# Performance work log

Measured on AMD Instinct MI355X. Metric: run time of the kernel, lower is better.

## Reference

```python
import jax, jax.numpy as jnp
import numpy as np

LN_EPS = 1e-5


def _ln(x, g, b):
    mu = jnp.mean(x, -1, keepdims=True)
    xc = x - mu
    inv = jax.lax.rsqrt(jnp.mean(xc * xc, -1, keepdims=True) + LN_EPS)
    return xc * inv * g + b


def _subm_conv(x, nbr, W, b):
    # Submanifold 3D conv via rulebook gather-GEMM-accumulate.
    # x: [N, Cin], nbr: [N, K] neighbor row ids (-1 = missing), W: [K, Cin, Cout], b: [Cout]
    N = x.shape[0]
    xp = jnp.concatenate([x, jnp.zeros((1, x.shape[1]), x.dtype)], 0)  # sentinel zero row
    idx = jnp.where(nbr < 0, N, nbr)  # missing neighbors -> zero row
    acc0 = jnp.zeros((N, W.shape[-1]), x.dtype) + b
    def body(acc, xs):
        i, Wk = xs  # i: [N], Wk: [Cin, Cout]
        return acc + xp[i] @ Wk, None
    acc, _ = jax.lax.scan(body, acc0, (idx.T, W))
    return acc


def _blk1(x, W, b, g, be):  # 1x1x1 SubMConv + LN + ReLU
    return jax.nn.relu(_ln(x @ W + b, g, be))


def _blk3(x, nbr, W, b, g, be):  # 3x3x3 SubMConv + LN + ReLU
    return jax.nn.relu(_ln(_subm_conv(x, nbr, W, b), g, be))


def setup_inputs() -> dict:
    rng = np.random.default_rng(0)
    B, D, Npb, K = 2, 160, 131072, 27
    dim, half = 64, 32
    # Build random sparse voxel set and the rulebook (neighbor table) like spconv does.
    lookup = np.full((B, D, D, D), -1, np.int64)
    coords = np.zeros((B * Npb, 3), np.int64)
    for b in range(B):
        lin = np.sort(rng.choice(D * D * D, size=Npb, replace=False))
        z, y, x = np.unravel_index(lin, (D, D, D))
        rows = np.arange(b * Npb, (b + 1) * Npb)
        lookup[b, z, y, x] = rows
        coords[rows] = np.stack([z, y, x], 1)
    bidx = np.repeat(np.arange(B), Npb)
    offs = np.stack(np.meshgrid(np.arange(-1, 2), np.arange(-1, 2), np.arange(-1, 2), indexing="ij"), -1).reshape(K, 3)
    nz = coords[:, None, :] + offs[None]  # [N, K, 3]
    valid = ((nz >= 0) & (nz < D)).all(-1)
    nzc = np.clip(nz, 0, D - 1)
    nbr = lookup[bidx[:, None], nzc[..., 0], nzc[..., 1], nzc[..., 2]]
    nbr = np.where(valid, nbr, -1).astype(np.int32)

    key = jax.random.key(0)
    ks = iter(jax.random.split(key, 16))
    f32 = jnp.float32
    d = {"voxel_features": jax.random.normal(next(ks), (B * Npb, dim), f32),
         "nbr_idx": jnp.asarray(nbr)}
    def lnp(c):
        return jnp.ones((c,), f32), jnp.zeros((c,), f32)
    d["W1"] = 0.05 * jax.random.normal(next(ks), (dim, dim), f32); d["b1"] = jnp.zeros((dim,), f32); d["g1"], d["be1"] = lnp(dim)
    d["W2"] = 0.05 * jax.random.normal(next(ks), (dim, dim), f32); d["b2"] = jnp.zeros((dim,), f32); d["g2"], d["be2"] = lnp(dim)
    d["W3"] = 0.05 * jax.random.normal(next(ks), (K, dim, half), f32); d["b3"] = jnp.zeros((half,), f32); d["g3"], d["be3"] = lnp(half)
    d["W4"] = 0.05 * jax.random.normal(next(ks), (K, half, half), f32); d["b4"] = jnp.zeros((half,), f32); d["g4"], d["be4"] = lnp(half)
    d["W5"] = 0.05 * jax.random.normal(next(ks), (K, half, half), f32); d["b5"] = jnp.zeros((half,), f32); d["g5"], d["be5"] = lnp(half)
    d["W6"] = 0.05 * jax.random.normal(next(ks), (K, half, half), f32); d["b6"] = jnp.zeros((half,), f32); d["g6"], d["be6"] = lnp(half)
    d["W7"] = 0.05 * jax.random.normal(next(ks), (4 * dim, dim), f32); d["b7"] = jnp.zeros((dim,), f32); d["g7"], d["be7"] = lnp(dim)
    return d


def reference(voxel_features, nbr_idx,
              W1, b1, g1, be1, W2, b2, g2, be2,
              W3, b3, g3, be3, W4, b4, g4, be4,
              W5, b5, g5, be5, W6, b6, g6, be6,
              W7, b7, g7, be7):
    x = voxel_features
    f1 = _blk1(x, W1, b1, g1, be1)
    f2 = _blk1(x, W2, b2, g2, be2)
    feats = [f1, f2]
    f2 = _blk3(f2, nbr_idx, W3, b3, g3, be3); feats.append(f2)
    f2 = _blk3(f2, nbr_idx, W4, b4, g4, be4); feats.append(f2)
    f2 = _blk3(f2, nbr_idx, W5, b5, g5, be5); feats.append(f2)
    f2 = _blk3(f2, nbr_idx, W6, b6, g6, be6); feats.append(f2)
    cat = jnp.concatenate(feats, -1)  # [N, 4*dim]
    return _blk1(cat, W7, b7, g7, be7)
```

## Files before the change

kernel.cpp:

```cpp
#include <hip/hip_runtime.h>

typedef __attribute__((ext_vector_type(4))) float  float4_;
typedef __attribute__((ext_vector_type(8))) short  short8;
typedef __attribute__((ext_vector_type(8))) __bf16 bf16x8;

__device__ inline unsigned short f2bf(float f) {
    unsigned u = __builtin_bit_cast(unsigned, f);
    u += 0x7FFFu + ((u >> 16) & 1u);
    return (unsigned short)(u >> 16);
}

__device__ inline float4_ mfma16(bf16x8 a, bf16x8 b, float4_ c) {
    return __builtin_amdgcn_mfma_f32_16x16x32_bf16(a, b, c, 0, 0, 0);
}

__device__ inline void packW_one(const float* __restrict__ src, unsigned short* __restrict__ dst,
                                 int cin, int cout, int e) {
    int f = e >> 9, i = e & 511, lane = i >> 3, t = i & 7;
    int ntn = cout >> 4, ctn = cin >> 5;
    int nt = f % ntn;
    int rest = f / ntn;
    int ct = rest % ctn;
    int k = rest / ctn;
    int c = ct * 32 + (lane >> 4) * 8 + t;
    int j = nt * 16 + (lane & 15);
    dst[e] = f2bf(src[(k * cin + c) * cout + j]);
}

__global__ void pack_all_kernel(
    const float* __restrict__ W1, const float* __restrict__ W2,
    const float* __restrict__ W3, const float* __restrict__ W4,
    const float* __restrict__ W5, const float* __restrict__ W6,
    const float* __restrict__ W7,
    unsigned short* cat, unsigned short* Wp12, unsigned short* Wp3,
    unsigned short* Wp4, unsigned short* Wp5, unsigned short* Wp6,
    unsigned short* Wp7, int N) {
    int e = blockIdx.x * 256 + threadIdx.x;
    if (e < 8192) {
        int f = e >> 9, i = e & 511, lane = i >> 3, t = i & 7;
        int nt = f & 7, ct = f >> 3;
        int c = ct * 32 + (lane >> 4) * 8 + t;
        int j = nt * 16 + (lane & 15);
        float v = (j < 64) ? W1[c * 64 + j] : W2[c * 64 + (j - 64)];
        Wp12[e] = f2bf(v);
        return;
    }
    e -= 8192;
    if (e < 55296) { packW_one(W3, Wp3, 64, 32, e); return; }
    e -= 55296;
    if (e < 27648) { packW_one(W4, Wp4, 32, 32, e); return; }
    e -= 27648;
    if (e < 27648) { packW_one(W5, Wp5, 32, 32, e); return; }
    e -= 27648;
    if (e < 27648) { packW_one(W6, Wp6, 32, 32, e); return; }
    e -= 27648;
    if (e < 16384) { packW_one(W7, Wp7, 256, 64, e); return; }
    e -= 16384;
    if (e < 128) ((unsigned*)(cat + (size_t)N * 256))[e] = 0;
}

__global__ __launch_bounds__(256) void plan_kernel(const int* __restrict__ nbr,
                                                   unsigned int* __restrict__ kmask) {
    __shared__ unsigned tm[16];
    int tid = threadIdx.x;
    if (tid < 16) tm[tid] = 0u;
    __syncthreads();
    long base = (long)blockIdx.x * 6912;
#pragma unroll
    for (int i = 0; i < 27; i++) {
        int j = i * 256 + tid;
        int v = nbr[base + j];
        if (v >= 0) {
            unsigned r = (unsigned)j / 27u;
            unsigned k = (unsigned)j - r * 27u;
            atomicOr(&tm[r >> 4], 1u << k);
        }
    }
    __syncthreads();
    if (tid < 16) kmask[blockIdx.x * 16 + tid] = tm[tid];
}

__global__ __launch_bounds__(256) void blk12_kernel(
    const float* __restrict__ x, unsigned short* cat,
    const unsigned short* __restrict__ Wp,
    const float* __restrict__ b1, const float* __restrict__ g1, const float* __restrict__ be1,
    const float* __restrict__ b2, const float* __restrict__ g2, const float* __restrict__ be2) {
    int tid = threadIdx.x, lane = tid & 63, wv = tid >> 6;
    int l15 = lane & 15, q = lane >> 4;
    long base = ((long)blockIdx.x * 4 + wv) * 16;

    float4_ acc[8];
#pragma unroll
    for (int i = 0; i < 8; i++) acc[i] = (float4_){0.f, 0.f, 0.f, 0.f};

#pragma unroll
    for (int kt = 0; kt < 2; kt++) {
        const float* xp = x + (base + l15) * 64 + kt * 32 + q * 8;
        float4_ f0 = *(const float4_*)xp;
        float4_ f1 = *(const float4_*)(xp + 4);
        short8 as;
        as[0] = (short)f2bf(f0[0]); as[1] = (short)f2bf(f0[1]);
        as[2] = (short)f2bf(f0[2]); as[3] = (short)f2bf(f0[3]);
        as[4] = (short)f2bf(f1[0]); as[5] = (short)f2bf(f1[1]);
        as[6] = (short)f2bf(f1[2]); as[7] = (short)f2bf(f1[3]);
        bf16x8 a = __builtin_bit_cast(bf16x8, as);
        const unsigned short* wp = Wp + (size_t)kt * 8 * 512;
#pragma unroll
        for (int nt = 0; nt < 8; nt++) {
            bf16x8 w = *(const bf16x8*)(wp + nt * 512 + lane * 8);
            acc[nt] = mfma16(a, w, acc[nt]);
        }
    }

    float bc[8], gc[8], bec[8];
#pragma unroll
    for (int nt = 0; nt < 8; nt++) {
        int j = nt * 16 + l15;
        if (j < 64) { bc[nt] = b1[j]; gc[nt] = g1[j]; bec[nt] = be1[j]; }
        else        { bc[nt] = b2[j - 64]; gc[nt] = g2[j - 64]; bec[nt] = be2[j - 64]; }
    }

#pragma unroll
    for (int r = 0; r < 4; r++) {
        long row = base + q * 4 + r;
        float v[8], s0 = 0.f, s1 = 0.f, q0 = 0.f, q1 = 0.f;
#pragma unroll
        for (int nt = 0; nt < 4; nt++) { v[nt] = acc[nt][r] + bc[nt]; s0 += v[nt]; q0 += v[nt] * v[nt]; }
#pragma unroll
        for (int nt = 4; nt < 8; nt++) { v[nt] = acc[nt][r] + bc[nt]; s1 += v[nt]; q1 += v[nt] * v[nt]; }
#pragma unroll
        for (int m = 1; m < 16; m <<= 1) {
            s0 += __shfl_xor(s0, m); q0 += __shfl_xor(q0, m);
            s1 += __shfl_xor(s1, m); q1 += __shfl_xor(q1, m);
        }
        float mu0 = s0 * (1.f / 64), var0 = q0 * (1.f / 64) - mu0 * mu0, inv0 = rsqrtf(var0 + 1e-5f);
        float mu1 = s1 * (1.f / 64), var1 = q1 * (1.f / 64) - mu1 * mu1, inv1 = rsqrtf(var1 + 1e-5f);
        unsigned short* cp = cat + row * 256;
#pragma unroll
        for (int nt = 0; nt < 4; nt++) {
            float y = fmaxf((v[nt] - mu0) * inv0 * gc[nt] + bec[nt], 0.f);
            cp[nt * 16 + l15] = f2bf(y);
        }
#pragma unroll
        for (int nt = 4; nt < 8; nt++) {
            float y = fmaxf((v[nt] - mu1) * inv1 * gc[nt] + bec[nt], 0.f);
            cp[nt * 16 + l15] = f2bf(y);
        }
    }
}

template <int CT, int D>
__global__ __launch_bounds__(256) void conv_kernel(
    unsigned short* cat, const int* __restrict__ nbr,
    const unsigned int* __restrict__ kmask,
    const unsigned short* __restrict__ Wp,
    const float* __restrict__ bb, const float* __restrict__ gg, const float* __restrict__ bee,
    int in_off, int out_off, int N) {
    int tid = threadIdx.x, lane = tid & 63, wv = tid >> 6;
    int l15 = lane & 15, q = lane >> 4;

    int cpx = (int)(gridDim.x >> 3);
    int sb = ((int)blockIdx.x & 7) * cpx + ((int)blockIdx.x >> 3);
    int t = sb * 4 + wv;
    long base = (long)t * 16;

    unsigned m = __builtin_amdgcn_readfirstlane(kmask[t]);

    float4_ acc[2];
    acc[0] = (float4_){0.f, 0.f, 0.f, 0.f};
    acc[1] = (float4_){0.f, 0.f, 0.f, 0.f};

    const unsigned short* catp = cat + in_off + q * 8;
    const unsigned short* wl = Wp + lane * 8;
    const int* np = nbr + (base + l15) * 27;

    bf16x8 f[D + 1][CT];
    bf16x8 wr[3][CT][2];
    int rawi[3];

    int raw0[D + 2];
#pragma unroll
    for (int j = 0; j < D + 2; j++) raw0[j] = (m >> j & 1u) ? np[j] : -1;

#pragma unroll
    for (int kk = 0; kk < 2; kk++) {
        if (m >> kk & 1u) {
#pragma unroll
            for (int ct = 0; ct < CT; ct++)
#pragma unroll
                for (int nt = 0; nt < 2; nt++)
                    wr[kk][ct][nt] =
                        *(const bf16x8*)(wl + ((size_t)((kk * CT + ct) * 2 + nt)) * 512);
        }
    }

#pragma unroll
    for (int j = 0; j < D; j++) {
        if (m >> j & 1u) {
            int v = raw0[j];
            size_t s = (size_t)(v < 0 ? N : v);
#pragma unroll
            for (int ct = 0; ct < CT; ct++)
                f[j][ct] = *(const bf16x8*)(catp + s * 256 + ct * 32);
        }
    }
    rawi[D % 3] = raw0[D];
    rawi[(D + 1) % 3] = raw0[D + 1];

#pragma unroll
    for (int k = 0; k < 27; k++) {
        if (k + 2 < 27 && (m >> (k + 2) & 1u)) {
#pragma unroll
            for (int ct = 0; ct < CT; ct++)
#pragma unroll
                for (int nt = 0; nt < 2; nt++)
                    wr[(k + 2) % 3][ct][nt] =
                        *(const bf16x8*)(wl + ((size_t)(((k + 2) * CT + ct) * 2 + nt)) * 512);
        }
        if (k + D < 27 && (m >> (k + D) & 1u)) {
            int v = rawi[(k + D) % 3];
            size_t s = (size_t)(v < 0 ? N : v);
#pragma unroll
            for (int ct = 0; ct < CT; ct++)
                f[(k + D) % (D + 1)][ct] = *(const bf16x8*)(catp + s * 256 + ct * 32);
        }
        if (k + D + 2 < 27 && (m >> (k + D + 2) & 1u)) {
            rawi[(k + D + 2) % 3] = np[k + D + 2];
        }
        if (m >> k & 1u) {
#pragma unroll
            for (int ct = 0; ct < CT; ct++) {
                bf16x8 w0 = wr[k % 3][ct][0];
                bf16x8 w1 = wr[k % 3][ct][1];
                acc[0] = mfma16(f[k % (D + 1)][ct], w0, acc[0]);
                acc[1] = mfma16(f[k % (D + 1)][ct], w1, acc[1]);
            }
        }
    }

    float b0c = bb[l15], b1c = bb[16 + l15];
    float g0c = gg[l15], g1c = gg[16 + l15];
    float be0c = bee[l15], be1c = bee[16 + l15];

#pragma unroll
    for (int r = 0; r < 4; r++) {
        long row = base + q * 4 + r;
        float v0 = acc[0][r] + b0c;
        float v1 = acc[1][r] + b1c;
        float s = v0 + v1, sq = v0 * v0 + v1 * v1;
#pragma unroll
        for (int mh = 1; mh < 16; mh <<= 1) { s += __shfl_xor(s, mh); sq += __shfl_xor(sq, mh); }
        float mu = s * (1.f / 32), var = sq * (1.f / 32) - mu * mu, inv = rsqrtf(var + 1e-5f);
        float y0 = fmaxf((v0 - mu) * inv * g0c + be0c, 0.f);
        float y1 = fmaxf((v1 - mu) * inv * g1c + be1c, 0.f);
        unsigned short* cp = cat + row * 256 + out_off;
        cp[l15] = f2bf(y0);
        cp[16 + l15] = f2bf(y1);
    }
}

__global__ __launch_bounds__(256) void blk7_kernel(
    const unsigned short* __restrict__ cat, const unsigned short* __restrict__ Wp,
    const float* __restrict__ b, const float* __restrict__ g, const float* __restrict__ be,
    float* __restrict__ out) {
    int tid = threadIdx.x, lane = tid & 63, wv = tid >> 6;
    int l15 = lane & 15, q = lane >> 4;
    long base = ((long)blockIdx.x * 4 + wv) * 16;

    float4_ acc[4];
#pragma unroll
    for (int i = 0; i < 4; i++) acc[i] = (float4_){0.f, 0.f, 0.f, 0.f};

#pragma unroll
    for (int kt = 0; kt < 8; kt++) {
        bf16x8 a = *(const bf16x8*)(cat + (base + l15) * 256 + kt * 32 + q * 8);
        const unsigned short* wp = Wp + (size_t)kt * 4 * 512;
#pragma unroll
        for (int nt = 0; nt < 4; nt++) {
            bf16x8 w = *(const bf16x8*)(wp + nt * 512 + lane * 8);
            acc[nt] = mfma16(a, w, acc[nt]);
        }
    }

    float bc[4], gc[4], bec[4];
#pragma unroll
    for (int nt = 0; nt < 4; nt++) {
        int j = nt * 16 + l15;
        bc[nt] = b[j]; gc[nt] = g[j]; bec[nt] = be[j];
    }

#pragma unroll
    for (int r = 0; r < 4; r++) {
        long row = base + q * 4 + r;
        float v[4], s = 0.f, sq = 0.f;
#pragma unroll
        for (int nt = 0; nt < 4; nt++) { v[nt] = acc[nt][r] + bc[nt]; s += v[nt]; sq += v[nt] * v[nt]; }
#pragma unroll
        for (int m = 1; m < 16; m <<= 1) { s += __shfl_xor(s, m); sq += __shfl_xor(sq, m); }
        float mu = s * (1.f / 64), var = sq * (1.f / 64) - mu * mu, inv = rsqrtf(var + 1e-5f);
#pragma unroll
        for (int nt = 0; nt < 4; nt++) {
            float y = fmaxf((v[nt] - mu) * inv * gc[nt] + bec[nt], 0.f);
            out[row * 64 + nt * 16 + l15] = y;
        }
    }
}

extern "C" void kernel_launch(void* const* d_in, const int* in_sizes, int n_in,
                              void* d_out, int out_size, void* d_ws, size_t ws_size,
                              hipStream_t stream) {
    const int N = in_sizes[0] / 64;

    const float* x   = (const float*)d_in[0];
    const int*   nbr = (const int*)d_in[1];
    const float* W1 = (const float*)d_in[2];
    const float* b1 = (const float*)d_in[3];
    const float* g1 = (const float*)d_in[4];
    const float* be1 = (const float*)d_in[5];
    const float* W2 = (const float*)d_in[6];
    const float* b2 = (const float*)d_in[7];
    const float* g2 = (const float*)d_in[8];
    const float* be2 = (const float*)d_in[9];
    const float* W3 = (const float*)d_in[10];
    const float* b3 = (const float*)d_in[11];
    const float* g3 = (const float*)d_in[12];
    const float* be3 = (const float*)d_in[13];
    const float* W4 = (const float*)d_in[14];
    const float* b4 = (const float*)d_in[15];
    const float* g4 = (const float*)d_in[16];
    const float* be4 = (const float*)d_in[17];
    const float* W5 = (const float*)d_in[18];
    const float* b5 = (const float*)d_in[19];
    const float* g5 = (const float*)d_in[20];
    const float* be5 = (const float*)d_in[21];
    const float* W6 = (const float*)d_in[22];
    const float* b6 = (const float*)d_in[23];
    const float* g6 = (const float*)d_in[24];
    const float* be6 = (const float*)d_in[25];
    const float* W7 = (const float*)d_in[26];
    const float* b7 = (const float*)d_in[27];
    const float* g7 = (const float*)d_in[28];
    const float* be7 = (const float*)d_in[29];

    unsigned short* ws   = (unsigned short*)d_ws;
    unsigned short* cat  = ws;
    unsigned short* Wp12 = cat + (size_t)(N + 1) * 256;
    unsigned short* Wp3  = Wp12 + 8192;
    unsigned short* Wp4  = Wp3 + 55296;
    unsigned short* Wp5  = Wp4 + 27648;
    unsigned short* Wp6  = Wp5 + 27648;
    unsigned short* Wp7  = Wp6 + 27648;
    unsigned int*   kmask = (unsigned int*)(Wp7 + 16384);

    pack_all_kernel<<<637, 256, 0, stream>>>(W1, W2, W3, W4, W5, W6, W7,
                                             cat, Wp12, Wp3, Wp4, Wp5, Wp6, Wp7, N);
    plan_kernel<<<N / 256, 256, 0, stream>>>(nbr, kmask);

    blk12_kernel<<<N / 64, 256, 0, stream>>>(x, cat, Wp12, b1, g1, be1, b2, g2, be2);
    conv_kernel<2, 6><<<N / 64, 256, 0, stream>>>(cat, nbr, kmask, Wp3, b3, g3, be3, 64, 128, N);
    conv_kernel<1, 10><<<N / 64, 256, 0, stream>>>(cat, nbr, kmask, Wp4, b4, g4, be4, 128, 160, N);
    conv_kernel<1, 10><<<N / 64, 256, 0, stream>>>(cat, nbr, kmask, Wp5, b5, g5, be5, 160, 192, N);
    conv_kernel<1, 10><<<N / 64, 256, 0, stream>>>(cat, nbr, kmask, Wp6, b6, g6, be6, 192, 224, N);
    blk7_kernel<<<N / 64, 256, 0, stream>>>(cat, Wp7, b7, g7, be7, (float*)d_out);
}
```

Baseline: 471.4 us.

## Compact active kernel offsets per tile into a transposed index list for conv

The plan kernel now builds, for each 16-row tile, a compacted and transposed list of neighbor indices covering only the kernel offsets that have at least one neighbor in the tile. Missing neighbors are mapped to the zero sentinel row. The conv kernels walk this dense list with branch-free loads of weights selected by each offset's real index, padding the tail with a zeroed weight slot. This removes per-offset mask branches and strided 27-int loads, and makes index loads coalesced. In exchange it adds an extra index buffer write and read, and prefetch depths are retuned to smaller values. Tiles with fewer than 27 active offsets still execute all 27 MFMA steps, using padded zero weights for the inactive ones.

```diff
diff --git a/kernel.cpp b/kernel.cpp
--- a/kernel.cpp
+++ b/kernel.cpp
@@ -46,21 +46,23 @@
         return;
     }
     e -= 8192;
-    if (e < 55296) { packW_one(W3, Wp3, 64, 32, e); return; }
-    e -= 55296;
-    if (e < 27648) { packW_one(W4, Wp4, 32, 32, e); return; }
-    e -= 27648;
-    if (e < 27648) { packW_one(W5, Wp5, 32, 32, e); return; }
-    e -= 27648;
-    if (e < 27648) { packW_one(W6, Wp6, 32, 32, e); return; }
-    e -= 27648;
+    if (e < 57344) { if (e < 55296) packW_one(W3, Wp3, 64, 32, e); else Wp3[e] = 0; return; }
+    e -= 57344;
+    if (e < 28672) { if (e < 27648) packW_one(W4, Wp4, 32, 32, e); else Wp4[e] = 0; return; }
+    e -= 28672;
+    if (e < 28672) { if (e < 27648) packW_one(W5, Wp5, 32, 32, e); else Wp5[e] = 0; return; }
+    e -= 28672;
+    if (e < 28672) { if (e < 27648) packW_one(W6, Wp6, 32, 32, e); else Wp6[e] = 0; return; }
+    e -= 28672;
     if (e < 16384) { packW_one(W7, Wp7, 256, 64, e); return; }
     e -= 16384;
     if (e < 128) ((unsigned*)(cat + (size_t)N * 256))[e] = 0;
 }
 
 __global__ __launch_bounds__(256) void plan_kernel(const int* __restrict__ nbr,
-                                                   unsigned int* __restrict__ kmask) {
+                                                   unsigned int* __restrict__ kmask,
+                                                   int* __restrict__ cidx, int N) {
+    __shared__ int snb[6912];
     __shared__ unsigned tm[16];
     int tid = threadIdx.x;
     if (tid < 16) tm[tid] = 0u;
@@ -70,6 +72,7 @@
     for (int i = 0; i < 27; i++) {
         int j = i * 256 + tid;
         int v = nbr[base + j];
+        snb[j] = v;
         if (v >= 0) {
             unsigned r = (unsigned)j / 27u;
             unsigned k = (unsigned)j - r * 27u;
@@ -77,7 +80,20 @@
         }
     }
     __syncthreads();
-    if (tid < 16) kmask[blockIdx.x * 16 + tid] = tm[tid];
+    int g = tid >> 4, r = tid & 15;
+    unsigned m = tm[g];
+    int t = blockIdx.x * 16 + g;
+    int* cp = cidx + (long)t * 432;
+    int j = 0;
+#pragma unroll
+    for (int k = 0; k < 27; k++) {
+        if (m >> k & 1u) {
+            int v = snb[(g * 16 + r) * 27 + k];
+            cp[j * 16 + r] = (v < 0) ? N : v;
+            j++;
+        }
+    }
+    if (r == 0) kmask[t] = m;
 }
 
 __global__ __launch_bounds__(256) void blk12_kernel(
@@ -151,7 +167,7 @@
 
 template <int CT, int D>
 __global__ __launch_bounds__(256) void conv_kernel(
-    unsigned short* cat, const int* __restrict__ nbr,
+    unsigned short* cat, const int* __restrict__ cidx,
     const unsigned int* __restrict__ kmask,
     const unsigned short* __restrict__ Wp,
     const float* __restrict__ bb, const float* __restrict__ gg, const float* __restrict__ bee,
@@ -166,75 +182,72 @@
 
     unsigned m = __builtin_amdgcn_readfirstlane(kmask[t]);
 
+    int ke[27];
+    unsigned mm = m;
+#pragma unroll
+    for (int j = 0; j < 27; j++) {
+        ke[j] = mm ? (int)__builtin_ctz(mm) : 27;
+        mm &= mm - 1u;
+    }
+
     float4_ acc[2];
     acc[0] = (float4_){0.f, 0.f, 0.f, 0.f};
     acc[1] = (float4_){0.f, 0.f, 0.f, 0.f};
 
     const unsigned short* catp = cat + in_off + q * 8;
     const unsigned short* wl = Wp + lane * 8;
-    const int* np = nbr + (base + l15) * 27;
+    const int* cx = cidx + (long)t * 432 + l15;
 
     bf16x8 f[D + 1][CT];
     bf16x8 wr[3][CT][2];
-    int rawi[3];
-
-    int raw0[D + 2];
-#pragma unroll
-    for (int j = 0; j < D + 2; j++) raw0[j] = (m >> j & 1u) ? np[j] : -1;
-
-#pragma unroll
-    for (int kk = 0; kk < 2; kk++) {
-        if (m >> kk & 1u) {
-#pragma unroll
-            for (int ct = 0; ct < CT; ct++)
-#pragma unroll
-                for (int nt = 0; nt < 2; nt++)
-                    wr[kk][ct][nt] =
-                        *(const bf16x8*)(wl + ((size_t)((kk * CT + ct) * 2 + nt)) * 512);
-        }
-    }
+    int ci[3];
+
+    int ci0[D + 2];
+#pragma unroll
+    for (int j = 0; j < D + 2; j++) ci0[j] = cx[j * 16];
+
+#pragma unroll
+    for (int kk = 0; kk < 2; kk++)
+#pragma unroll
+        for (int ct = 0; ct < CT; ct++)
+#pragma unroll
+            for (int nt = 0; nt < 2; nt++)
+                wr[kk][ct][nt] =
+                    *(const bf16x8*)(wl + ((size_t)((ke[kk] * CT + ct) * 2 + nt)) * 512);
 
 #pragma unroll
     for (int j = 0; j < D; j++) {
-        if (m >> j & 1u) {
-            int v = raw0[j];
-            size_t s = (size_t)(v < 0 ? N : v);
-#pragma unroll
-            for (int ct = 0; ct < CT; ct++)
-                f[j][ct] = *(const bf16x8*)(catp + s * 256 + ct * 32);
-        }
-    }
-    rawi[D % 3] = raw0[D];
-    rawi[(D + 1) % 3] = raw0[D + 1];
+        int v = ci0[j];
+        size_t s = (size_t)(v < 0 ? 0 : (v > N ? N : v));
+#pragma unroll
+        for (int ct = 0; ct < CT; ct++)
+            f[j][ct] = *(const bf16x8*)(catp + s * 256 + ct * 32);
+    }
+    ci[D % 3] = ci0[D];
+    ci[(D + 1) % 3] = ci0[D + 1];
 
 #pragma unroll
     for (int k = 0; k < 27; k++) {
-        if (k + 2 < 27 && (m >> (k + 2) & 1u)) {
+        if (k + 2 < 27) {
 #pragma unroll
             for (int ct = 0; ct < CT; ct++)
 #pragma unroll
                 for (int nt = 0; nt < 2; nt++)
                     wr[(k + 2) % 3][ct][nt] =
-                        *(const bf16x8*)(wl + ((size_t)(((k + 2) * CT + ct) * 2 + nt)) * 512);
-        }
-        if (k + D < 27 && (m >> (k + D) & 1u)) {
-            int v = rawi[(k + D) % 3];
-            size_t s = (size_t)(v < 0 ? N : v);
+                        *(const bf16x8*)(wl + ((size_t)((ke[k + 2] * CT + ct) * 2 + nt)) * 512);
+        }
+        if (k + D < 27) {
+            int v = ci[(k + D) % 3];
+            size_t s = (size_t)(v < 0 ? 0 : (v > N ? N : v));
 #pragma unroll
             for (int ct = 0; ct < CT; ct++)
                 f[(k + D) % (D + 1)][ct] = *(const bf16x8*)(catp + s * 256 + ct * 32);
         }
-        if (k + D + 2 < 27 && (m >> (k + D + 2) & 1u)) {
-            rawi[(k + D + 2) % 3] = np[k + D + 2];
-        }
-        if (m >> k & 1u) {
-#pragma unroll
-            for (int ct = 0; ct < CT; ct++) {
-                bf16x8 w0 = wr[k % 3][ct][0];
-                bf16x8 w1 = wr[k % 3][ct][1];
-                acc[0] = mfma16(f[k % (D + 1)][ct], w0, acc[0]);
-                acc[1] = mfma16(f[k % (D + 1)][ct], w1, acc[1]);
-            }
+        if (k + D + 2 < 27) ci[(k + D + 2) % 3] = cx[(k + D + 2) * 16];
+#pragma unroll
+        for (int ct = 0; ct < CT; ct++) {
+            acc[0] = mfma16(f[k % (D + 1)][ct], wr[k % 3][ct][0], acc[0]);
+            acc[1] = mfma16(f[k % (D + 1)][ct], wr[k % 3][ct][1], acc[1]);
         }
     }
 
@@ -346,20 +359,21 @@
     unsigned short* cat  = ws;
     unsigned short* Wp12 = cat + (size_t)(N + 1) * 256;
     unsigned short* Wp3  = Wp12 + 8192;
-    unsigned short* Wp4  = Wp3 + 55296;
-    unsigned short* Wp5  = Wp4 + 27648;
-    unsigned short* Wp6  = Wp5 + 27648;
-    unsigned short* Wp7  = Wp6 + 27648;
+    unsigned short* Wp4  = Wp3 + 57344;
+    unsigned short* Wp5  = Wp4 + 28672;
+    unsigned short* Wp6  = Wp5 + 28672;
+    unsigned short* Wp7  = Wp6 + 28672;
     unsigned int*   kmask = (unsigned int*)(Wp7 + 16384);
-
-    pack_all_kernel<<<637, 256, 0, stream>>>(W1, W2, W3, W4, W5, W6, W7,
+    int*            cidx  = (int*)(kmask + N / 16);
+
+    pack_all_kernel<<<657, 256, 0, stream>>>(W1, W2, W3, W4, W5, W6, W7,
                                              cat, Wp12, Wp3, Wp4, Wp5, Wp6, Wp7, N);
-    plan_kernel<<<N / 256, 256, 0, stream>>>(nbr, kmask);
+    plan_kernel<<<N / 256, 256, 0, stream>>>(nbr, kmask, cidx, N);
 
     blk12_kernel<<<N / 64, 256, 0, stream>>>(x, cat, Wp12, b1, g1, be1, b2, g2, be2);
-    conv_kernel<2, 6><<<N / 64, 256, 0, stream>>>(cat, nbr, kmask, Wp3, b3, g3, be3, 64, 128, N);
-    conv_kernel<1, 10><<<N / 64, 256, 0, stream>>>(cat, nbr, kmask, Wp4, b4, g4, be4, 128, 160, N);
-    conv_kernel<1, 10><<<N / 64, 256, 0, stream>>>(cat, nbr, kmask, Wp5, b5, g5, be5, 160, 192, N);
-    conv_kernel<1, 10><<<N / 64, 256, 0, stream>>>(cat, nbr, kmask, Wp6, b6, g6, be6, 192, 224, N);
+    conv_kernel<2, 3><<<N / 64, 256, 0, stream>>>(cat, cidx, kmask, Wp3, b3, g3, be3, 64, 128, N);
+    conv_kernel<1, 4><<<N / 64, 256, 0, stream>>>(cat, cidx, kmask, Wp4, b4, g4, be4, 128, 160, N);
+    conv_kernel<1, 4><<<N / 64, 256, 0, stream>>>(cat, cidx, kmask, Wp5, b5, g5, be5, 160, 192, N);
+    conv_kernel<1, 4><<<N / 64, 256, 0, stream>>>(cat, cidx, kmask, Wp6, b6, g6, be6, 192, 224, N);
     blk7_kernel<<<N / 64, 256, 0, stream>>>(cat, Wp7, b7, g7, be7, (float*)d_out);
 }
```

Result: slower. 524.5 us (+11.3%).

## Precompute coalesced byte-offset neighbor table and optionally stage conv weights in LDS

Applied to the files above, without the earlier changes.

The plan kernel now also writes a transposed per-tile table of byte offsets (missing neighbors mapped to the zero row), so conv kernels read neighbor indices coalesced, 16 lanes per offset, with no per-load select or multiply. Conv kernels gain a template flag that copies the packed weights into shared memory once per block; it is enabled only for the second conv layer. Prefetch depths drop from 6/10 to 3/4. This trades an extra table written once and reused across four convs, plus LDS pressure, for cheaper index loads, at the risk of exposing gather latency through the shallower prefetch.

```diff
diff --git a/kernel.cpp b/kernel.cpp
--- a/kernel.cpp
+++ b/kernel.cpp
@@ -60,7 +60,9 @@
 }
 
 __global__ __launch_bounds__(256) void plan_kernel(const int* __restrict__ nbr,
-                                                   unsigned int* __restrict__ kmask) {
+                                                   unsigned int* __restrict__ kmask,
+                                                   unsigned int* __restrict__ cidx, int N) {
+    __shared__ int snb[6912];
     __shared__ unsigned tm[16];
     int tid = threadIdx.x;
     if (tid < 16) tm[tid] = 0u;
@@ -70,6 +72,7 @@
     for (int i = 0; i < 27; i++) {
         int j = i * 256 + tid;
         int v = nbr[base + j];
+        snb[j] = v;
         if (v >= 0) {
             unsigned r = (unsigned)j / 27u;
             unsigned k = (unsigned)j - r * 27u;
@@ -77,7 +80,15 @@
         }
     }
     __syncthreads();
-    if (tid < 16) kmask[blockIdx.x * 16 + tid] = tm[tid];
+    int g = tid >> 4, r = tid & 15;
+    int t = blockIdx.x * 16 + g;
+    unsigned* cp = cidx + (long)t * 432;
+#pragma unroll
+    for (int k = 0; k < 27; k++) {
+        int v = snb[(g * 16 + r) * 27 + k];
+        cp[k * 16 + r] = (unsigned)((v < 0 ? N : v)) * 512u;
+    }
+    if (r == 0) kmask[t] = tm[g];
 }
 
 __global__ __launch_bounds__(256) void blk12_kernel(
@@ -149,15 +160,28 @@
     }
 }
 
-template <int CT, int D>
+template <int CT, int D, int LDSW>
 __global__ __launch_bounds__(256) void conv_kernel(
-    unsigned short* cat, const int* __restrict__ nbr,
+    unsigned short* cat, const unsigned int* __restrict__ cidx,
     const unsigned int* __restrict__ kmask,
     const unsigned short* __restrict__ Wp,
     const float* __restrict__ bb, const float* __restrict__ gg, const float* __restrict__ bee,
     int in_off, int out_off, int N) {
+    __shared__ unsigned short wlds[LDSW ? 27648 : 16];
     int tid = threadIdx.x, lane = tid & 63, wv = tid >> 6;
     int l15 = lane & 15, q = lane >> 4;
+
+    if (LDSW) {
+        const unsigned* src = (const unsigned*)Wp;
+        unsigned* dst = (unsigned*)wlds;
+#pragma unroll
+        for (int i = 0; i < 54; i++) dst[i * 256 + tid] = src[i * 256 + tid];
+        __syncthreads();
+    }
+
+#define WLOAD(KK, CTI, NT)                                                             \
+    (LDSW ? *(const bf16x8*)(wlds + ((size_t)(((KK) * CT + (CTI)) * 2 + (NT))) * 512 + lane * 8) \
+          : *(const bf16x8*)(Wp   + ((size_t)(((KK) * CT + (CTI)) * 2 + (NT))) * 512 + lane * 8))
 
     int cpx = (int)(gridDim.x >> 3);
     int sb = ((int)blockIdx.x & 7) * cpx + ((int)blockIdx.x >> 3);
@@ -170,17 +194,16 @@
     acc[0] = (float4_){0.f, 0.f, 0.f, 0.f};
     acc[1] = (float4_){0.f, 0.f, 0.f, 0.f};
 
-    const unsigned short* catp = cat + in_off + q * 8;
-    const unsigned short* wl = Wp + lane * 8;
-    const int* np = nbr + (base + l15) * 27;
+    const char* catb = (const char*)cat + (size_t)in_off * 2 + q * 16;
+    const unsigned* cx = cidx + (long)t * 432 + l15;
 
     bf16x8 f[D + 1][CT];
     bf16x8 wr[3][CT][2];
-    int rawi[3];
-
-    int raw0[D + 2];
-#pragma unroll
-    for (int j = 0; j < D + 2; j++) raw0[j] = (m >> j & 1u) ? np[j] : -1;
+    unsigned ci[3];
+
+    unsigned ci0[D + 2];
+#pragma unroll
+    for (int j = 0; j < D + 2; j++) ci0[j] = (m >> j & 1u) ? cx[j * 16] : 0u;
 
 #pragma unroll
     for (int kk = 0; kk < 2; kk++) {
@@ -189,23 +212,20 @@
             for (int ct = 0; ct < CT; ct++)
 #pragma unroll
                 for (int nt = 0; nt < 2; nt++)
-                    wr[kk][ct][nt] =
-                        *(const bf16x8*)(wl + ((size_t)((kk * CT + ct) * 2 + nt)) * 512);
+                    wr[kk][ct][nt] = WLOAD(kk, ct, nt);
         }
     }
 
 #pragma unroll
     for (int j = 0; j < D; j++) {
         if (m >> j & 1u) {
-            int v = raw0[j];
-            size_t s = (size_t)(v < 0 ? N : v);
 #pragma unroll
             for (int ct = 0; ct < CT; ct++)
-                f[j][ct] = *(const bf16x8*)(catp + s * 256 + ct * 32);
-        }
-    }
-    rawi[D % 3] = raw0[D];
-    rawi[(D + 1) % 3] = raw0[D + 1];
+                f[j][ct] = *(const bf16x8*)(catb + (size_t)ci0[j] + ct * 64);
+        }
+    }
+    ci[D % 3] = ci0[D];
+    ci[(D + 1) % 3] = ci0[D + 1];
 
 #pragma unroll
     for (int k = 0; k < 27; k++) {
@@ -214,18 +234,16 @@
             for (int ct = 0; ct < CT; ct++)
 #pragma unroll
                 for (int nt = 0; nt < 2; nt++)
-                    wr[(k + 2) % 3][ct][nt] =
-                        *(const bf16x8*)(wl + ((size_t)(((k + 2) * CT + ct) * 2 + nt)) * 512);
+                    wr[(k + 2) % 3][ct][nt] = WLOAD(k + 2, ct, nt);
         }
         if (k + D < 27 && (m >> (k + D) & 1u)) {
-            int v = rawi[(k + D) % 3];
-            size_t s = (size_t)(v < 0 ? N : v);
+            unsigned voff = ci[(k + D) % 3];
 #pragma unroll
             for (int ct = 0; ct < CT; ct++)
-                f[(k + D) % (D + 1)][ct] = *(const bf16x8*)(catp + s * 256 + ct * 32);
+                f[(k + D) % (D + 1)][ct] = *(const bf16x8*)(catb + (size_t)voff + ct * 64);
         }
         if (k + D + 2 < 27 && (m >> (k + D + 2) & 1u)) {
-            rawi[(k + D + 2) % 3] = np[k + D + 2];
+            ci[(k + D + 2) % 3] = cx[(k + D + 2) * 16];
         }
         if (m >> k & 1u) {
 #pragma unroll
@@ -237,6 +255,7 @@
             }
         }
     }
+#undef WLOAD
 
     float b0c = bb[l15], b1c = bb[16 + l15];
     float g0c = gg[l15], g1c = gg[16 + l15];
@@ -351,15 +370,16 @@
     unsigned short* Wp6  = Wp5 + 27648;
     unsigned short* Wp7  = Wp6 + 27648;
     unsigned int*   kmask = (unsigned int*)(Wp7 + 16384);
+    unsigned int*   cidx  = kmask + N / 16;
 
     pack_all_kernel<<<637, 256, 0, stream>>>(W1, W2, W3, W4, W5, W6, W7,
                                              cat, Wp12, Wp3, Wp4, Wp5, Wp6, Wp7, N);
-    plan_kernel<<<N / 256, 256, 0, stream>>>(nbr, kmask);
+    plan_kernel<<<N / 256, 256, 0, stream>>>(nbr, kmask, cidx, N);
 
     blk12_kernel<<<N / 64, 256, 0, stream>>>(x, cat, Wp12, b1, g1, be1, b2, g2, be2);
-    conv_kernel<2, 6><<<N / 64, 256, 0, stream>>>(cat, nbr, kmask, Wp3, b3, g3, be3, 64, 128, N);
-    conv_kernel<1, 10><<<N / 64, 256, 0, stream>>>(cat, nbr, kmask, Wp4, b4, g4, be4, 128, 160, N);
-    conv_kernel<1, 10><<<N / 64, 256, 0, stream>>>(cat, nbr, kmask, Wp5, b5, g5, be5, 160, 192, N);
-    conv_kernel<1, 10><<<N / 64, 256, 0, stream>>>(cat, nbr, kmask, Wp6, b6, g6, be6, 192, 224, N);
+    conv_kernel<2, 3, 0><<<N / 64, 256, 0, stream>>>(cat, cidx, kmask, Wp3, b3, g3, be3, 64, 128, N);
+    conv_kernel<1, 4, 1><<<N / 64, 256, 0, stream>>>(cat, cidx, kmask, Wp4, b4, g4, be4, 128, 160, N);
+    conv_kernel<1, 4, 0><<<N / 64, 256, 0, stream>>>(cat, cidx, kmask, Wp5, b5, g5, be5, 160, 192, N);
+    conv_kernel<1, 4, 0><<<N / 64, 256, 0, stream>>>(cat, cidx, kmask, Wp6, b6, g6, be6, 192, 224, N);
     blk7_kernel<<<N / 64, 256, 0, stream>>>(cat, Wp7, b7, g7, be7, (float*)d_out);
 }
```

After: 523.6 us. +11.1%, slower.
